# Kernel tuning notes

Hardware: AMD Instinct MI355X
Metric: run time of the kernel (lower is better)

The kernel has to match this reference:

```python
import jax, jax.numpy as jnp
import numpy as np

BRANCH = 4
DEPTH = 5
D = 512
N_NODES = (BRANCH ** (DEPTH + 1) - 1) // (BRANCH - 1)  # 1365
BATCH = 16


def setup_inputs() -> dict:
    key = jax.random.key(0)
    k1, k2, k3 = jax.random.split(key, 3)
    inputs = jax.random.normal(k1, (BATCH, D), dtype=jnp.float32)
    # per-node Linear(512,512) weights, torch layout [out, in], scaled like kaiming-ish init
    W = jax.random.normal(k2, (N_NODES, D, D), dtype=jnp.float32) * (1.0 / np.sqrt(D))
    b = jax.random.normal(k3, (N_NODES, D), dtype=jnp.float32) * 0.01
    return {"inputs": inputs, "W": W, "b": b}


def reference(inputs, W, b):
    # BFS over a complete BRANCH-ary tree; node i>0 has parent (i-1)//BRANCH.
    # Root: Linear only (no relu, per source); children: relu(Linear(parent_act)).
    # All nodes at one BFS level are batched into a single grouped einsum.
    acts = []
    a = inputs @ W[0].T + b[0]          # [B, D] root, no relu
    acts.append(a[:, None, :])
    prev = acts[0]                       # [B, level_size, D]
    prev_start = 0
    start = 1
    for lvl in range(1, DEPTH + 1):
        sz = BRANCH ** lvl
        idx = np.arange(start, start + sz)
        parent_local = (idx - 1) // BRANCH - prev_start  # indices into prev level
        pa = prev[:, parent_local, :]                    # [B, sz, D]
        Wl = W[start:start + sz]                         # [sz, D(out), D(in)]
        bl = b[start:start + sz]                         # [sz, D]
        a = jax.nn.relu(jnp.einsum('bnd,nhd->bnh', pa, Wl) + bl)  # [B, sz, D]
        acts.append(a)
        prev = a
        prev_start = start
        start += sz
    out = jnp.concatenate(acts, axis=1)                  # [B, N_NODES, D]
    return out.reshape(out.shape[0], -1)                 # [B, N_NODES*D], like torch.cat(dim=1)
```

## Files before the change

### kernel.cpp

```cpp
#include <hip/hip_runtime.h>

#define D 512
#define NNODES 1365
#define OUT_STRIDE (NNODES * D)

typedef __attribute__((ext_vector_type(4))) float f32x4;
typedef __attribute__((ext_vector_type(8))) short bf16x8;

union U4 { unsigned u[4]; bf16x8 v; };

__device__ __forceinline__ unsigned cvt_pk_bf16(float s0, float s1) {
    unsigned r;
    asm volatile("v_cvt_pk_bf16_f32 %0, %1, %2" : "=v"(r) : "v"(s0), "v"(s1));
    return r;
}

__device__ __forceinline__ void gld_lds16(const void* g, void* l) {
    __builtin_amdgcn_global_load_lds(
        (const __attribute__((address_space(1))) unsigned*)g,
        (__attribute__((address_space(3))) unsigned*)l, 16, 0, 0);
}

template<int N> __device__ __forceinline__ void waitV() {
    asm volatile("s_waitcnt vmcnt(%0)" :: "i"(N) : "memory");
}

__device__ __forceinline__ void mfma3(bf16x8 ah, bf16x8 al, f32x4 b0, f32x4 b1,
                                      f32x4& acc) {
    U4 bH, bL;
    float xs[8] = {b0[0],b0[1],b0[2],b0[3],b1[0],b1[1],b1[2],b1[3]};
    #pragma unroll
    for (int k = 0; k < 4; ++k) {
        unsigned hh = cvt_pk_bf16(xs[2*k], xs[2*k+1]);
        float f0 = __uint_as_float(hh << 16);
        float f1 = __uint_as_float(hh & 0xFFFF0000u);
        bL.u[k] = cvt_pk_bf16(xs[2*k] - f0, xs[2*k+1] - f1);
        bH.u[k] = hh;
    }
    acc = __builtin_amdgcn_mfma_f32_16x16x32_bf16(ah, bH.v, acc, 0,0,0);
    acc = __builtin_amdgcn_mfma_f32_16x16x32_bf16(al, bH.v, acc, 0,0,0);
    acc = __builtin_amdgcn_mfma_f32_16x16x32_bf16(ah, bL.v, acc, 0,0,0);
}

__device__ __forceinline__ void build_afrags(const float* arow, int m4,
                                             bf16x8* aH, bf16x8* aL) {
    #pragma unroll
    for (int j = 0; j < 16; ++j) {
        const float* p = arow + j * 32 + m4 * 8;
        f32x4 x0 = *(const f32x4*)p;
        f32x4 x1 = *(const f32x4*)(p + 4);
        float xs[8] = {x0[0],x0[1],x0[2],x0[3],x1[0],x1[1],x1[2],x1[3]};
        U4 h, l;
        #pragma unroll
        for (int k = 0; k < 4; ++k) {
            unsigned hh = cvt_pk_bf16(xs[2*k], xs[2*k+1]);
            float f0 = __uint_as_float(hh << 16);
            float f1 = __uint_as_float(hh & 0xFFFF0000u);
            l.u[k] = cvt_pk_bf16(xs[2*k] - f0, xs[2*k+1] - f1);
            h.u[k] = hh;
        }
        aH[j] = h.v; aL[j] = l.v;
    }
}

template<int NGW>
__global__ __launch_bounds__(256)
void reg_kernel(const float* __restrict__ W, const float* __restrict__ bias,
                const float* __restrict__ src, float* __restrict__ out,
                int node_start, int bpn)
{
    const int tid  = threadIdx.x;
    const int w    = tid >> 6;
    const int lane = tid & 63;
    const int m4   = lane >> 4;
    const int c0   = lane & 15;

    const int node  = node_start + blockIdx.x / bpn;
    const int nbase = (blockIdx.x % bpn) * (64 * NGW) + w * (16 * NGW);
    const char* Wn  = (const char*)(W + (size_t)node * (D * D));

    const float* arow = src + (size_t)c0 * OUT_STRIDE
                            + (size_t)((node - 1) >> 2) * D;
    bf16x8 aH[16], aL[16];
    build_afrags(arow, m4, aH, aL);

    const char*  lanebase = Wn + (size_t)(nbase + c0) * 2048 + m4 * 32;
    const float* bptr     = bias + (size_t)node * D + nbase + c0;
    float*       optr     = out  + (size_t)node * D + nbase + c0;

    #pragma clang loop unroll(disable)
    for (int g = 0; g < NGW; ++g) {
        const char* gb = lanebase + (size_t)g * 32768;
        const float bv = bptr[g * 16];
        f32x4 acc = {0.f, 0.f, 0.f, 0.f};
        #pragma unroll
        for (int q = 0; q < 4; ++q) {
            f32x4 r0[4], r1[4];
            #pragma unroll
            for (int k = 0; k < 4; ++k) {
                r0[k] = *(const f32x4*)(gb + q * 512 + k * 128);
                r1[k] = *(const f32x4*)(gb + q * 512 + k * 128 + 16);
            }
            #pragma unroll
            for (int k = 0; k < 4; ++k)
                mfma3(aH[q * 4 + k], aL[q * 4 + k], r0[k], r1[k], acc);
        }
        #pragma unroll
        for (int i = 0; i < 4; ++i)
            optr[(size_t)(m4 * 4 + i) * OUT_STRIDE + g * 16] =
                fmaxf(acc[i] + bv, 0.f);
    }
}

template<bool RELU>
__global__ __launch_bounds__(256, 2)
void node_kernel(const float* __restrict__ W, const float* __restrict__ bias,
                 const float* __restrict__ src_base, float* __restrict__ out,
                 int node_start, int bpn, int ngroups, int src_stride)
{
    __shared__ float Wt[4][2][2048];
    __shared__ float bias_lds[512];

    const int tid  = threadIdx.x;
    const int w    = tid >> 6;
    const int lane = tid & 63;
    const int m4   = lane >> 4;
    const int c0   = lane & 15;

    const int node  = node_start + blockIdx.x / bpn;
    const int nbase = (blockIdx.x % bpn) * (64 * ngroups);
    const char* Wn  = (const char*)(W + (size_t)node * (D * D));

    for (int t = tid; t < 64 * ngroups; t += 256)
        bias_lds[t] = bias[(size_t)node * D + nbase + t];

    const float* arow = (RELU ? src_base + (size_t)((node - 1) >> 2) * D
                              : src_base) + (size_t)c0 * src_stride;
    bf16x8 aH[16], aL[16];
    build_afrags(arow, m4, aH, aL);
    __syncthreads();

    int loffs[8];
    const int rr  = lane >> 5;
    const int off = (lane & 31) * 16;
    #pragma unroll
    for (int i = 0; i < 8; ++i) {
        const int r = i * 2 + rr;
        loffs[i] = r * 2048 + (off ^ ((r & 7) << 4));
    }
    auto issue = [&](const char* gsrc, int buf) {
        char* ldst = (char*)&Wt[w][buf][0];
        #pragma unroll
        for (int i = 0; i < 8; ++i)
            gld_lds16(gsrc + loffs[i], ldst + i * 1024);
    };

    const int rsw = (c0 & 7) << 4;
    const int po0 = c0 * 512 + ((m4 * 32)      ^ rsw);
    const int po1 = c0 * 512 + ((m4 * 32 + 16) ^ rsw);

    const size_t GRP = (size_t)64 * 2048;
    const char* gcur = Wn + (size_t)(nbase + w * 16) * 2048;
    issue(gcur,       0);
    issue(gcur + 512, 1);

    float* optr = out + (size_t)node * D + nbase + w * 16 + c0;
    const float* blds = &bias_lds[w * 16 + c0];

    auto compute_q = [&](auto qc, f32x4& acc) {
        constexpr int Q = decltype(qc)::value;
        const char* tb = (const char*)&Wt[w][Q & 1][0];
        #pragma unroll
        for (int ks = 0; ks < 4; ++ks) {
            f32x4 b0 = *(const f32x4*)(tb + po0 + ks * 128);
            f32x4 b1 = *(const f32x4*)(tb + po1 + ks * 128);
            mfma3(aH[Q*4+ks], aL[Q*4+ks], b0, b1, acc);
        }
    };

    #pragma clang loop unroll(disable)
    for (int g = 0; g < ngroups; ++g) {
        const bool last = (g == ngroups - 1);
        const char* gnext = gcur + GRP;
        f32x4 acc = {0.f,0.f,0.f,0.f};

        waitV<8>();
        compute_q(std::integral_constant<int,0>{}, acc);
        issue(gcur + 1024, 0);
        waitV<8>();
        compute_q(std::integral_constant<int,1>{}, acc);
        issue(gcur + 1536, 1);
        waitV<8>();
        compute_q(std::integral_constant<int,2>{}, acc);
        if (!last) issue(gnext, 0);
        if (last) waitV<0>(); else waitV<8>();
        compute_q(std::integral_constant<int,3>{}, acc);

        const float bv = *blds;
        #pragma unroll
        for (int i = 0; i < 4; ++i) {
            float v = acc[i] + bv;
            if (RELU) v = fmaxf(v, 0.f);
            optr[(size_t)(m4 * 4 + i) * OUT_STRIDE] = v;
        }
        if (!last) issue(gnext + 512, 1);

        gcur = gnext; optr += 64; blds += 64;
    }
}

extern "C" void kernel_launch(void* const* d_in, const int* in_sizes, int n_in,
                              void* d_out, int out_size, void* d_ws, size_t ws_size,
                              hipStream_t stream) {
    const float* inputs = (const float*)d_in[0];
    const float* W      = (const float*)d_in[1];
    const float* bias   = (const float*)d_in[2];
    float* out          = (float*)d_out;

    node_kernel<false><<<   8, 256, 0, stream>>>(W, bias, inputs, out,   0, 8, 1, D);
    node_kernel<true ><<<  32, 256, 0, stream>>>(W, bias, out,    out,   1, 8, 1, OUT_STRIDE);
    node_kernel<true ><<< 128, 256, 0, stream>>>(W, bias, out,    out,   5, 8, 1, OUT_STRIDE);
    node_kernel<true ><<< 512, 256, 0, stream>>>(W, bias, out,    out,  21, 8, 1, OUT_STRIDE);
    reg_kernel<4><<< 512, 256, 0, stream>>>(W, bias, out, out,  85, 2);
    reg_kernel<8><<<1024, 256, 0, stream>>>(W, bias, out, out, 341, 1);
}
```

Before: 362.1 us.

## Replace register-direct weight loads with LDS-staged persistent sweep for last levels

Level 4 now uses the LDS double-buffered node_kernel instead of the register-load kernel. The last level (1024 nodes) gets a new persistent sweep kernel: 512 blocks loop over 16 work items each, streaming weights through swizzled LDS buffers via global_load_lds. The aim is better memory-level parallelism and coalescing on the dominant weight stream. The cost is that A fragments are rebuilt for every item, and the pipeline drains at the end of each item because the next item's loads are not prefetched.

After: 382.8 us. 1.06x slower.

```diff
diff --git a/kernel.cpp b/kernel.cpp
--- a/kernel.cpp
+++ b/kernel.cpp
@@ -1,4 +1,5 @@
 #include <hip/hip_runtime.h>
+#include <type_traits>
 
 #define D 512
 #define NNODES 1365
@@ -63,51 +64,75 @@
     }
 }
 
-template<int NGW>
-__global__ __launch_bounds__(256)
-void reg_kernel(const float* __restrict__ W, const float* __restrict__ bias,
-                const float* __restrict__ src, float* __restrict__ out,
-                int node_start, int bpn)
+__global__ __launch_bounds__(256, 2)
+void sweep_kernel(const float* __restrict__ W, const float* __restrict__ bias,
+                  const float* __restrict__ src, float* __restrict__ out,
+                  int node_start, int T, int nblk)
 {
+    __shared__ float Wt[4][2][2048];
+
     const int tid  = threadIdx.x;
     const int w    = tid >> 6;
     const int lane = tid & 63;
     const int m4   = lane >> 4;
     const int c0   = lane & 15;
 
-    const int node  = node_start + blockIdx.x / bpn;
-    const int nbase = (blockIdx.x % bpn) * (64 * NGW) + w * (16 * NGW);
-    const char* Wn  = (const char*)(W + (size_t)node * (D * D));
-
-    const float* arow = src + (size_t)c0 * OUT_STRIDE
-                            + (size_t)((node - 1) >> 2) * D;
+    int loffs[8];
+    const int rr  = lane >> 5;
+    const int off = (lane & 31) * 16;
+    #pragma unroll
+    for (int i = 0; i < 8; ++i) {
+        const int r = i * 2 + rr;
+        loffs[i] = r * 2048 + (off ^ ((r & 7) << 4));
+    }
+    const int rsw = (c0 & 7) << 4;
+    const int po0 = c0 * 512 + ((m4 * 32)      ^ rsw);
+    const int po1 = c0 * 512 + ((m4 * 32 + 16) ^ rsw);
+
+    auto issue = [&](const char* g, int buf) {
+        char* l = (char*)&Wt[w][buf][0];
+        #pragma unroll
+        for (int i = 0; i < 8; ++i)
+            gld_lds16(g + loffs[i], l + i * 1024);
+    };
+
     bf16x8 aH[16], aL[16];
-    build_afrags(arow, m4, aH, aL);
-
-    const char*  lanebase = Wn + (size_t)(nbase + c0) * 2048 + m4 * 32;
-    const float* bptr     = bias + (size_t)node * D + nbase + c0;
-    float*       optr     = out  + (size_t)node * D + nbase + c0;
+    auto cq = [&](auto qc, f32x4& acc) {
+        constexpr int Q = decltype(qc)::value;
+        const char* tb = (const char*)&Wt[w][Q & 1][0];
+        #pragma unroll
+        for (int ks = 0; ks < 4; ++ks) {
+            f32x4 b0 = *(const f32x4*)(tb + po0 + ks * 128);
+            f32x4 b1 = *(const f32x4*)(tb + po1 + ks * 128);
+            mfma3(aH[Q*4+ks], aL[Q*4+ks], b0, b1, acc);
+        }
+    };
 
     #pragma clang loop unroll(disable)
-    for (int g = 0; g < NGW; ++g) {
-        const char* gb = lanebase + (size_t)g * 32768;
-        const float bv = bptr[g * 16];
+    for (int t = 0; t < T; ++t) {
+        const int item    = t * nblk + blockIdx.x;
+        const int node    = node_start + (item >> 3);
+        const int rowbase = (item & 7) * 64 + w * 16;
+        const char* gb = (const char*)W
+            + (size_t)node * (D * D * 4) + (size_t)rowbase * 2048;
+
+        const float* arow = src + (size_t)c0 * OUT_STRIDE
+                                + (size_t)((node - 1) >> 2) * D;
+        build_afrags(arow, m4, aH, aL);
+        const float bv = bias[(size_t)node * D + rowbase + c0];
+
+        issue(gb,       0);
+        issue(gb + 512, 1);
         f32x4 acc = {0.f, 0.f, 0.f, 0.f};
-        #pragma unroll
-        for (int q = 0; q < 4; ++q) {
-            f32x4 r0[4], r1[4];
-            #pragma unroll
-            for (int k = 0; k < 4; ++k) {
-                r0[k] = *(const f32x4*)(gb + q * 512 + k * 128);
-                r1[k] = *(const f32x4*)(gb + q * 512 + k * 128 + 16);
-            }
-            #pragma unroll
-            for (int k = 0; k < 4; ++k)
-                mfma3(aH[q * 4 + k], aL[q * 4 + k], r0[k], r1[k], acc);
-        }
+        waitV<8>(); cq(std::integral_constant<int,0>{}, acc); issue(gb + 1024, 0);
+        waitV<8>(); cq(std::integral_constant<int,1>{}, acc); issue(gb + 1536, 1);
+        waitV<8>(); cq(std::integral_constant<int,2>{}, acc);
+        waitV<0>(); cq(std::integral_constant<int,3>{}, acc);
+
+        const int wcol = node * D + rowbase + c0;
         #pragma unroll
         for (int i = 0; i < 4; ++i)
-            optr[(size_t)(m4 * 4 + i) * OUT_STRIDE + g * 16] =
+            out[(size_t)(m4 * 4 + i) * OUT_STRIDE + wcol] =
                 fmaxf(acc[i] + bv, 0.f);
     }
 }
@@ -221,6 +246,6 @@
     node_kernel<true ><<<  32, 256, 0, stream>>>(W, bias, out,    out,   1, 8, 1, OUT_STRIDE);
     node_kernel<true ><<< 128, 256, 0, stream>>>(W, bias, out,    out,   5, 8, 1, OUT_STRIDE);
     node_kernel<true ><<< 512, 256, 0, stream>>>(W, bias, out,    out,  21, 8, 1, OUT_STRIDE);
-    reg_kernel<4><<< 512, 256, 0, stream>>>(W, bias, out, out,  85, 2);
-    reg_kernel<8><<<1024, 256, 0, stream>>>(W, bias, out, out, 341, 1);
-}
+    node_kernel<true ><<< 512, 256, 0, stream>>>(W, bias, out,    out,  85, 2, 4, OUT_STRIDE);
+    sweep_kernel<<<512, 256, 0, stream>>>(W, bias, out, out, 341, 16, 512);
+}
```
